# Optimization experiments

Hardware: AMD Instinct MI355X
Metric: run time of the kernel (lower is better)

Reference implementation:

```python
import jax, jax.numpy as jnp
import numpy as np

B, T, C = 2, 2048, 1024
H, D = 16, 64          # n_heads, head_dim
E, K, HD = 8, 2, 1536  # num_experts, active_experts, expert hidden (int(1.5*C))
EPS = 1e-6


def setup_inputs() -> dict:
    key = jax.random.key(0)
    ks = jax.random.split(key, 13)
    s = 0.02
    return {
        "x": jax.random.normal(ks[0], (B, T, C), jnp.float32),
        "rope_cos": jax.random.uniform(ks[1], (T, D), jnp.float32),
        "rope_sin": jax.random.uniform(ks[2], (T, D), jnp.float32),
        "attn_norm_w": jnp.ones((C,), jnp.float32),
        "q_w": jax.random.normal(ks[3], (C, C), jnp.float32) * s,
        "k_w": jax.random.normal(ks[4], (C, C), jnp.float32) * s,
        "v_w": jax.random.normal(ks[5], (C, C), jnp.float32) * s,
        "o_w": jax.random.normal(ks[6], (C, C), jnp.float32) * s,
        "ffn_norm_w": jnp.ones((C,), jnp.float32),
        "router_w": jax.random.normal(ks[7], (E, C), jnp.float32) * s,
        "w1": jax.random.normal(ks[8], (E, HD, C), jnp.float32) * s,
        "w2": jax.random.normal(ks[9], (E, C, HD), jnp.float32) * s,
        "w3": jax.random.normal(ks[10], (E, HD, C), jnp.float32) * s,
    }


def rmsnorm(x, w):
    var = jnp.mean(x * x, axis=-1, keepdims=True)
    return w * x * jax.lax.rsqrt(var + EPS)


def apply_rope(x, cos, sin):
    # x: [B, T, H, D]; cos/sin: [T, D]
    cos = cos[None, :, None, :]
    sin = sin[None, :, None, :]
    d = x.shape[-1] // 2
    x1, x2 = x[..., :d], x[..., d:]
    rotated = jnp.concatenate([-x2, x1], axis=-1)
    return x * cos + rotated * sin


def reference(x, rope_cos, rope_sin, attn_norm_w, q_w, k_w, v_w, o_w,
              ffn_norm_w, router_w, w1, w2, w3):
    b, t, c = x.shape
    h = rmsnorm(x, attn_norm_w)
    q = (h @ q_w.T).reshape(b, t, H, D)
    k = (h @ k_w.T).reshape(b, t, H, D)
    v = (h @ v_w.T).reshape(b, t, H, D)
    q = apply_rope(q, rope_cos[:t], rope_sin[:t]).transpose(0, 2, 1, 3)  # [B,H,T,D]
    k = apply_rope(k, rope_cos[:t], rope_sin[:t]).transpose(0, 2, 1, 3)
    v = v.transpose(0, 2, 1, 3)
    scores = jnp.einsum('bhqd,bhkd->bhqk', q, k) / jnp.sqrt(jnp.asarray(D, q.dtype))
    causal = jnp.tril(jnp.ones((t, t), bool))
    scores = jnp.where(causal, scores, -jnp.inf)
    attn = jax.nn.softmax(scores, axis=-1)
    y = jnp.einsum('bhqk,bhkd->bhqd', attn, v)
    y = y.transpose(0, 2, 1, 3).reshape(b, t, c)
    x = x + y @ o_w.T

    # Sparse MoE (top-K routing, per-expert SwiGLU, weighted combine)
    hn = rmsnorm(x, ffn_norm_w)
    flat = hn.reshape(-1, c)                                # [N, C]
    logits = flat @ router_w.T                              # [N, E]
    wk, idx = jax.lax.top_k(logits, K)                      # [N, K]
    wk = jax.nn.softmax(wk, axis=-1)
    # combined per-expert gate: [N, E] (zero for unrouted experts)
    gate = jnp.sum((idx[..., None] == jnp.arange(E)) * wk[..., None], axis=1)
    out = jnp.zeros_like(flat)
    for e in range(E):
        g = jax.nn.silu(flat @ w1[e].T) * (flat @ w3[e].T)  # [N, HD]
        out = out + gate[:, e:e + 1] * (g @ w2[e].T)
    return x + out.reshape(b, t, c)
```

## Files before the change

### kernel.cpp

```cpp
#include <hip/hip_runtime.h>
#include <hip/hip_bf16.h>
#include <math.h>

#define Bq 2
#define Tq 2048
#define Cq 1024
#define Hq 16
#define Dq 64
#define Eq 8
#define HDq 1536
#define NTOK (Bq*Tq)

typedef unsigned short u16;
typedef _Float16 f16;
typedef __bf16 bf16x8 __attribute__((ext_vector_type(8)));
typedef _Float16 f16x8 __attribute__((ext_vector_type(8)));
typedef float f32x4v __attribute__((ext_vector_type(4)));

#define MB(x) ((size_t)(x) * 262144)

__device__ __forceinline__ float silu_f(float a) {
    return a / (1.0f + __expf(-a));
}
__device__ __forceinline__ u16 f2bf(float f) {
    union { float f; unsigned u; } a; a.f = f;
    unsigned r = a.u + 0x7fffu + ((a.u >> 16) & 1u);
    return (u16)(r >> 16);
}
__device__ __forceinline__ u16 f16bits(f16 h) {
    union { f16 f; u16 u; } a; a.f = h; return a.u;
}

__device__ __forceinline__ void stage16(const void* g, void* l) {
    __builtin_amdgcn_global_load_lds(
        (const __attribute__((address_space(1))) unsigned int*)g,
        (__attribute__((address_space(3))) unsigned int*)l, 16, 0, 0);
}

__global__ __launch_bounds__(256) void rmsnorm_split_k(const float* __restrict__ x,
                                                       const float* __restrict__ w,
                                                       u16* __restrict__ hh,
                                                       u16* __restrict__ hl) {
    int row = blockIdx.x;
    int tid = threadIdx.x;
    const float* xr = x + (size_t)row * Cq;
    float4 v = *(const float4*)(xr + tid * 4);
    float ss = v.x*v.x + v.y*v.y + v.z*v.z + v.w*v.w;
    #pragma unroll
    for (int off = 32; off; off >>= 1) ss += __shfl_xor(ss, off);
    __shared__ float red[4];
    if ((tid & 63) == 0) red[tid >> 6] = ss;
    __syncthreads();
    float tot = red[0] + red[1] + red[2] + red[3];
    float scale = rsqrtf(tot * (1.0f / (float)Cq) + 1e-6f);
    float4 wv = *(const float4*)(w + tid * 4);
    float o[4] = { v.x*wv.x*scale, v.y*wv.y*scale, v.z*wv.z*scale, v.w*wv.w*scale };
    ushort4 oh, ol;
    u16* ph = (u16*)&oh; u16* pl = (u16*)&ol;
    #pragma unroll
    for (int i = 0; i < 4; i++) {
        f16 hi = (f16)o[i]; f16 lo = (f16)(o[i] - (float)hi);
        ph[i] = f16bits(hi); pl[i] = f16bits(lo);
    }
    *(ushort4*)(hh + (size_t)row * Cq + tid * 4) = oh;
    *(ushort4*)(hl + (size_t)row * Cq + tid * 4) = ol;
}

__global__ __launch_bounds__(256) void rmsnorm2_k(const float* __restrict__ x,
                                                  const float* __restrict__ w,
                                                  float* __restrict__ hn,
                                                  u16* __restrict__ hnb) {
    int row = blockIdx.x;
    int tid = threadIdx.x;
    const float* xr = x + (size_t)row * Cq;
    float4 v = *(const float4*)(xr + tid * 4);
    float ss = v.x*v.x + v.y*v.y + v.z*v.z + v.w*v.w;
    #pragma unroll
    for (int off = 32; off; off >>= 1) ss += __shfl_xor(ss, off);
    __shared__ float red[4];
    if ((tid & 63) == 0) red[tid >> 6] = ss;
    __syncthreads();
    float tot = red[0] + red[1] + red[2] + red[3];
    float scale = rsqrtf(tot * (1.0f / (float)Cq) + 1e-6f);
    float4 wv = *(const float4*)(w + tid * 4);
    float4 o = make_float4(v.x*wv.x*scale, v.y*wv.y*scale, v.z*wv.z*scale, v.w*wv.w*scale);
    *(float4*)(hn + (size_t)row * Cq + tid * 4) = o;
    ushort4 ob = make_ushort4(f2bf(o.x), f2bf(o.y), f2bf(o.z), f2bf(o.w));
    *(ushort4*)(hnb + (size_t)row * Cq + tid * 4) = ob;
}

__global__ __launch_bounds__(256) void wconv_k(const float* __restrict__ w1,
                                               const float* __restrict__ w3,
                                               const float* __restrict__ w2,
                                               u16* __restrict__ w1b,
                                               u16* __restrict__ w3b,
                                               u16* __restrict__ w2b) {
    int a = blockIdx.y;
    const float* src = (a == 0) ? w1 : ((a == 1) ? w3 : w2);
    u16* dst = (a == 0) ? w1b : ((a == 1) ? w3b : w2b);
    size_t i = ((size_t)blockIdx.x * 256 + threadIdx.x) * 8;
    float4 f0 = *(const float4*)(src + i);
    float4 f1 = *(const float4*)(src + i + 4);
    ushort4 o0 = make_ushort4(f2bf(f0.x), f2bf(f0.y), f2bf(f0.z), f2bf(f0.w));
    ushort4 o1 = make_ushort4(f2bf(f1.x), f2bf(f1.y), f2bf(f1.z), f2bf(f1.w));
    *(ushort4*)(dst + i)     = o0;
    *(ushort4*)(dst + i + 4) = o1;
}

__global__ __launch_bounds__(256, 3) void gemm_fused(const u16* __restrict__ Ahg,
                                                     const u16* __restrict__ Alg,
                                                     const float* __restrict__ Wq,
                                                     const float* __restrict__ Wk,
                                                     const float* __restrict__ Wv,
                                                     u16* __restrict__ qh_o,
                                                     u16* __restrict__ ql_o,
                                                     u16* __restrict__ kh_o,
                                                     u16* __restrict__ kl_o,
                                                     float* __restrict__ vf_o,
                                                     const float* __restrict__ cosb,
                                                     const float* __restrict__ sinb,
                                                     const float* __restrict__ aux,
                                                     float* __restrict__ outf,
                                                     int kind) {
    __shared__ u16 AhS[2][128*32], AlS[2][128*32], BhS[128*32], BlS[128*32];
    int tid = threadIdx.x;
    int wave = tid >> 6, lane = tid & 63;
    int wm = wave >> 1, wn = wave & 1;
    int bx = blockIdx.x, by = blockIdx.y;
    int proj, nx;
    const float* W;
    if (kind == 0) {
        proj = bx >> 3; nx = bx & 7;
        W = (proj == 0) ? Wq : ((proj == 1) ? Wk : Wv);
    } else {
        proj = 3; nx = bx; W = Wq;
    }

    int srow = tid >> 2, sch = (tid & 3) * 8;
    const u16* A0 = Ahg + (size_t)(by*128 + srow) * Cq + sch;
    const u16* A1 = A0 + (size_t)64 * Cq;
    const u16* L0 = Alg + (size_t)(by*128 + srow) * Cq + sch;
    const u16* L1 = L0 + (size_t)64 * Cq;
    const float* W0 = W + (size_t)(nx*128 + srow) * Cq + sch;
    const float* W1 = W0 + (size_t)64 * Cq;
    int lo0 = srow*32 + sch, lo1 = lo0 + 2048;

    f32x4v acc[4][4];
    #pragma unroll
    for (int i = 0; i < 4; i++)
        #pragma unroll
        for (int j = 0; j < 4; j++)
            #pragma unroll
            for (int r = 0; r < 4; r++) acc[i][j][r] = 0.0f;

    float wr0[8], wr1[8];
    stage16(A0, &AhS[0][lo0]);
    stage16(A1, &AhS[0][lo1]);
    stage16(L0, &AlS[0][lo0]);
    stage16(L1, &AlS[0][lo1]);
    *(float4*)&wr0[0] = *(const float4*)(W0);
    *(float4*)&wr0[4] = *(const float4*)(W0 + 4);
    *(float4*)&wr1[0] = *(const float4*)(W1);
    *(float4*)&wr1[4] = *(const float4*)(W1 + 4);

    int fr = lane & 15, fk = (lane >> 4) * 8;
    int cur = 0;
    for (int k0 = 0; k0 < Cq; k0 += 32, cur ^= 1) {
        __syncthreads();
        {
            f16x8 bh0, bl0, bh1, bl1;
            #pragma unroll
            for (int i = 0; i < 8; i++) {
                f16 h0 = (f16)wr0[i]; bh0[i] = h0; bl0[i] = (f16)(wr0[i] - (float)h0);
                f16 h1 = (f16)wr1[i]; bh1[i] = h1; bl1[i] = (f16)(wr1[i] - (float)h1);
            }
            *(f16x8*)(void*)&BhS[lo0] = bh0;
            *(f16x8*)(void*)&BlS[lo0] = bl0;
            *(f16x8*)(void*)&BhS[lo1] = bh1;
            *(f16x8*)(void*)&BlS[lo1] = bl1;
        }
        __syncthreads();
        int kn = k0 + 32;
        if (kn < Cq) {
            stage16(A0 + kn, &AhS[cur^1][lo0]);
            stage16(A1 + kn, &AhS[cur^1][lo1]);
            stage16(L0 + kn, &AlS[cur^1][lo0]);
            stage16(L1 + kn, &AlS[cur^1][lo1]);
            *(float4*)&wr0[0] = *(const float4*)(W0 + kn);
            *(float4*)&wr0[4] = *(const float4*)(W0 + kn + 4);
            *(float4*)&wr1[0] = *(const float4*)(W1 + kn);
            *(float4*)&wr1[4] = *(const float4*)(W1 + kn + 4);
        }
        f16x8 ah[4], al[4];
        #pragma unroll
        for (int mi = 0; mi < 4; mi++) {
            ah[mi] = *(const f16x8*)(const void*)&AhS[cur][(wm*64 + mi*16 + fr)*32 + fk];
            al[mi] = *(const f16x8*)(const void*)&AlS[cur][(wm*64 + mi*16 + fr)*32 + fk];
        }
        #pragma unroll
        for (int ni = 0; ni < 4; ni++) {
            f16x8 bhf = *(const f16x8*)(const void*)&BhS[(wn*64 + ni*16 + fr)*32 + fk];
            f16x8 blf = *(const f16x8*)(const void*)&BlS[(wn*64 + ni*16 + fr)*32 + fk];
            #pragma unroll
            for (int mi = 0; mi < 4; mi++) {
                acc[mi][ni] = __builtin_amdgcn_mfma_f32_16x16x32_f16(ah[mi], bhf, acc[mi][ni], 0, 0, 0);
                acc[mi][ni] = __builtin_amdgcn_mfma_f32_16x16x32_f16(ah[mi], blf, acc[mi][ni], 0, 0, 0);
                acc[mi][ni] = __builtin_amdgcn_mfma_f32_16x16x32_f16(al[mi], bhf, acc[mi][ni], 0, 0, 0);
            }
        }
    }

    int cr = (lane >> 4) * 4, cc = lane & 15;
    if (proj < 2) {
        u16* dh = (proj == 0) ? qh_o : kh_o;
        u16* dl = (proj == 0) ? ql_o : kl_o;
        float scale = (proj == 0) ? 0.125f : 1.0f;
        int hd = (nx * 2 + wn) * 64;
        #pragma unroll
        for (int mi = 0; mi < 4; mi++)
            #pragma unroll
            for (int r = 0; r < 4; r++) {
                int row = by*128 + wm*64 + mi*16 + cr + r;
                int t = row & (Tq - 1);
                #pragma unroll
                for (int ni = 0; ni < 2; ni++) {
                    int d0 = ni*16 + cc;
                    float a = acc[mi][ni][r];
                    float b = acc[mi][ni+2][r];
                    float c0 = cosb[t*Dq + d0],      s0 = sinb[t*Dq + d0];
                    float c1 = cosb[t*Dq + d0 + 32], s1 = sinb[t*Dq + d0 + 32];
                    float oa = (a * c0 - b * s0) * scale;
                    float ob = (b * c1 + a * s1) * scale;
                    size_t off = (size_t)row * Cq + hd + d0;
                    f16 ha = (f16)oa;
                    f16 hb = (f16)ob;
                    dh[off]      = f16bits(ha);
                    dl[off]      = f16bits((f16)(oa - (float)ha));
                    dh[off + 32] = f16bits(hb);
                    dl[off + 32] = f16bits((f16)(ob - (float)hb));
                }
            }
    } else if (proj == 2) {
        #pragma unroll
        for (int mi = 0; mi < 4; mi++)
            #pragma unroll
            for (int r = 0; r < 4; r++) {
                int row = by*128 + wm*64 + mi*16 + cr + r;
                #pragma unroll
                for (int ni = 0; ni < 4; ni++)
                    vf_o[(size_t)row * Cq + nx*128 + wn*64 + ni*16 + cc] = acc[mi][ni][r];
            }
    } else {
        #pragma unroll
        for (int mi = 0; mi < 4; mi++)
            #pragma unroll
            for (int r = 0; r < 4; r++) {
                int row = by*128 + wm*64 + mi*16 + cr + r;
                #pragma unroll
                for (int ni = 0; ni < 4; ni++) {
                    size_t off = (size_t)row * Cq + nx*128 + wn*64 + ni*16 + cc;
                    outf[off] = acc[mi][ni][r] + aux[off];
                }
            }
    }
}

__global__ __launch_bounds__(256) void vtrans_k(const float* __restrict__ v,
                                                u16* __restrict__ vth,
                                                u16* __restrict__ vtl) {
    __shared__ u16 Th[64 * 72];
    __shared__ u16 Tl[64 * 72];
    int tc = blockIdx.x;
    int bh = blockIdx.y;
    int b = bh >> 4, h = bh & 15;
    int tid = threadIdx.x;
    int tr = tid >> 2;
    int dc = (tid & 3) * 16;
    size_t gin = ((size_t)(b * Tq + tc * 64 + tr)) * Cq + h * Dq + dc;
    #pragma unroll
    for (int i = 0; i < 16; i += 4) {
        float4 f = *(const float4*)(v + gin + i);
        float fv[4] = {f.x, f.y, f.z, f.w};
        #pragma unroll
        for (int j = 0; j < 4; j++) {
            f16 hi = (f16)fv[j];
            f16 lo = (f16)(fv[j] - (float)hi);
            Th[(dc + i + j) * 72 + tr] = f16bits(hi);
            Tl[(dc + i + j) * 72 + tr] = f16bits(lo);
        }
    }
    __syncthreads();
    int dr = tid >> 2;
    int cc = (tid & 3) * 16;
    size_t gout = ((size_t)(bh * 64 + dr)) * Tq + tc * 64 + cc;
    *(uint4*)(vth + gout)     = *(uint4*)(Th + dr * 72 + cc);
    *(uint4*)(vth + gout + 8) = *(uint4*)(Th + dr * 72 + cc + 8);
    *(uint4*)(vtl + gout)     = *(uint4*)(Tl + dr * 72 + cc);
    *(uint4*)(vtl + gout + 8) = *(uint4*)(Tl + dr * 72 + cc + 8);
}

#define AST 72
__global__ __launch_bounds__(256, 2) void attn_f16(const u16* __restrict__ qh_g,
                                                   const u16* __restrict__ ql_g,
                                                   const u16* __restrict__ kh_g,
                                                   const u16* __restrict__ kl_g,
                                                   const u16* __restrict__ vth_g,
                                                   const u16* __restrict__ vtl_g,
                                                   u16* __restrict__ yh_g,
                                                   u16* __restrict__ yl_g) {
    __shared__ u16 Qh[64*AST], Ql[64*AST];
    __shared__ u16 Kh[64*AST], Kl[64*AST];
    __shared__ u16 Vh[64*AST], Vl[64*AST];
    __shared__ u16 Ph[64*AST], Pl[64*AST];

    int j  = blockIdx.x;
    int bh = blockIdx.y;
    int b = bh >> 4, h = bh & 15;
    int tid = threadIdx.x;
    int wv = tid >> 6, lane = tid & 63;
    int fr = lane & 15, fg = lane >> 4;
    int sr = tid >> 2, sc = (tid & 3) * 16;
    int aoff = (wv * 16 + fr) * AST + fg * 8;

    uint4 rkh0, rkh1, rkl0, rkl1, rvh0, rvh1, rvl0, rvl1;
    auto ldkv = [&](int kt) {
        size_t kg = ((size_t)(b * Tq + kt * 64 + sr)) * Cq + h * Dq + sc;
        size_t vg = ((size_t)(bh * 64 + sr)) * Tq + kt * 64 + sc;
        rkh0 = *(const uint4*)(kh_g + kg);  rkh1 = *(const uint4*)(kh_g + kg + 8);
        rkl0 = *(const uint4*)(kl_g + kg);  rkl1 = *(const uint4*)(kl_g + kg + 8);
        rvh0 = *(const uint4*)(vth_g + vg); rvh1 = *(const uint4*)(vth_g + vg + 8);
        rvl0 = *(const uint4*)(vtl_g + vg); rvl1 = *(const uint4*)(vtl_g + vg + 8);
    };

    #pragma unroll
    for (int pass = 0; pass < 2; pass++) {
        int qt = pass == 0 ? (31 - j) : j;

        __syncthreads();
        {
            size_t g = ((size_t)(b * Tq + qt * 64 + sr)) * Cq + h * Dq + sc;
            *(uint4*)(Qh + sr*AST + sc)     = *(const uint4*)(qh_g + g);
            *(uint4*)(Qh + sr*AST + sc + 8) = *(const uint4*)(qh_g + g + 8);
            *(uint4*)(Ql + sr*AST + sc)     = *(const uint4*)(ql_g + g);
            *(uint4*)(Ql + sr*AST + sc + 8) = *(const uint4*)(ql_g + g + 8);
        }
        ldkv(0);

        f32x4v acc_o[4];
        float m_i[4], l_i[4];
        #pragma unroll
        for (int i = 0; i < 4; i++) {
            m_i[i] = -1e30f; l_i[i] = 0.0f;
            #pragma unroll
            for (int r = 0; r < 4; r++) acc_o[i][r] = 0.0f;
        }

        for (int kt = 0; kt <= qt; kt++) {
            __syncthreads();
            *(uint4*)(Kh + sr*AST + sc)     = rkh0;
            *(uint4*)(Kh + sr*AST + sc + 8) = rkh1;
            *(uint4*)(Kl + sr*AST + sc)     = rkl0;
            *(uint4*)(Kl + sr*AST + sc + 8) = rkl1;
            *(uint4*)(Vh + sr*AST + sc)     = rvh0;
            *(uint4*)(Vh + sr*AST + sc + 8) = rvh1;
            *(uint4*)(Vl + sr*AST + sc)     = rvl0;
            *(uint4*)(Vl + sr*AST + sc + 8) = rvl1;
            __syncthreads();
            if (kt < qt) ldkv(kt + 1);

            f16x8 aqh0 = *(const f16x8*)(const void*)(Qh + aoff);
            f16x8 aqh1 = *(const f16x8*)(const void*)(Qh + aoff + 32);
            f16x8 aql0 = *(const f16x8*)(const void*)(Ql + aoff);
            f16x8 aql1 = *(const f16x8*)(const void*)(Ql + aoff + 32);

            f32x4v s[4];
            #pragma unroll
            for (int ni = 0; ni < 4; ni++) {
                int boff = (ni * 16 + fr) * AST + fg * 8;
                f16x8 kh0 = *(const f16x8*)(const void*)(Kh + boff);
                f16x8 kh1 = *(const f16x8*)(const void*)(Kh + boff + 32);
                f16x8 kl0 = *(const f16x8*)(const void*)(Kl + boff);
                f16x8 kl1 = *(const f16x8*)(const void*)(Kl + boff + 32);
                f32x4v t;
                #pragma unroll
                for (int r = 0; r < 4; r++) t[r] = 0.0f;
                t = __builtin_amdgcn_mfma_f32_16x16x32_f16(aqh0, kh0, t, 0, 0, 0);
                t = __builtin_amdgcn_mfma_f32_16x16x32_f16(aqh1, kh1, t, 0, 0, 0);
                t = __builtin_amdgcn_mfma_f32_16x16x32_f16(aqh0, kl0, t, 0, 0, 0);
                t = __builtin_amdgcn_mfma_f32_16x16x32_f16(aqh1, kl1, t, 0, 0, 0);
                t = __builtin_amdgcn_mfma_f32_16x16x32_f16(aql0, kh0, t, 0, 0, 0);
                t = __builtin_amdgcn_mfma_f32_16x16x32_f16(aql1, kh1, t, 0, 0, 0);
                s[ni] = t;
            }

            if (kt == qt) {
                #pragma unroll
                for (int ni = 0; ni < 4; ni++) {
                    int col = ni * 16 + fr;
                    #pragma unroll
                    for (int r = 0; r < 4; r++) {
                        int row = wv * 16 + fg * 4 + r;
                        if (col > row) s[ni][r] = -1e30f;
                    }
                }
            }

            float p[4][4];
            #pragma unroll
            for (int r = 0; r < 4; r++) {
                float mx = fmaxf(fmaxf(s[0][r], s[1][r]), fmaxf(s[2][r], s[3][r]));
                #pragma unroll
                for (int off = 1; off < 16; off <<= 1)
                    mx = fmaxf(mx, __shfl_xor(mx, off, 16));
                float mn = fmaxf(m_i[r], mx);
                float rs = 0.0f;
                #pragma unroll
                for (int ni = 0; ni < 4; ni++) {
                    p[ni][r] = __expf(s[ni][r] - mn);
                    rs += p[ni][r];
                }
                #pragma unroll
                for (int off = 1; off < 16; off <<= 1)
                    rs += __shfl_xor(rs, off, 16);
                float alpha = __expf(m_i[r] - mn);
                l_i[r] = l_i[r] * alpha + rs;
                m_i[r] = mn;
                #pragma unroll
                for (int ni = 0; ni < 4; ni++) acc_o[ni][r] *= alpha;
            }

            #pragma unroll
            for (int ni = 0; ni < 4; ni++) {
                #pragma unroll
                for (int r = 0; r < 4; r++) {
                    int off = (wv * 16 + fg * 4 + r) * AST + ni * 16 + fr;
                    f16 ph = (f16)p[ni][r];
                    f16 pl = (f16)(p[ni][r] - (float)ph);
                    Ph[off] = f16bits(ph);
                    Pl[off] = f16bits(pl);
                }
            }

            f16x8 aph0 = *(const f16x8*)(const void*)(Ph + aoff);
            f16x8 aph1 = *(const f16x8*)(const void*)(Ph + aoff + 32);
            f16x8 apl0 = *(const f16x8*)(const void*)(Pl + aoff);
            f16x8 apl1 = *(const f16x8*)(const void*)(Pl + aoff + 32);
            #pragma unroll
            for (int ni = 0; ni < 4; ni++) {
                int boff = (ni * 16 + fr) * AST + fg * 8;
                f16x8 vh0 = *(const f16x8*)(const void*)(Vh + boff);
                f16x8 vh1 = *(const f16x8*)(const void*)(Vh + boff + 32);
                f16x8 vl0 = *(const f16x8*)(const void*)(Vl + boff);
                f16x8 vl1 = *(const f16x8*)(const void*)(Vl + boff + 32);
                f32x4v t = acc_o[ni];
                t = __builtin_amdgcn_mfma_f32_16x16x32_f16(aph0, vh0, t, 0, 0, 0);
                t = __builtin_amdgcn_mfma_f32_16x16x32_f16(aph1, vh1, t, 0, 0, 0);
                t = __builtin_amdgcn_mfma_f32_16x16x32_f16(aph0, vl0, t, 0, 0, 0);
                t = __builtin_amdgcn_mfma_f32_16x16x32_f16(aph1, vl1, t, 0, 0, 0);
                t = __builtin_amdgcn_mfma_f32_16x16x32_f16(apl0, vh0, t, 0, 0, 0);
                t = __builtin_amdgcn_mfma_f32_16x16x32_f16(apl1, vh1, t, 0, 0, 0);
                acc_o[ni] = t;
            }
        }

        #pragma unroll
        for (int r = 0; r < 4; r++) {
            float inv = 1.0f / l_i[r];
            int row = qt * 64 + wv * 16 + fg * 4 + r;
            size_t base = ((size_t)(b * Tq + row)) * Cq + h * Dq + fr;
            #pragma unroll
            for (int ni = 0; ni < 4; ni++) {
                float yv = acc_o[ni][r] * inv;
                f16 hi = (f16)yv;
                f16 lo = (f16)(yv - (float)hi);
                yh_g[base + ni * 16] = f16bits(hi);
                yl_g[base + ni * 16] = f16bits(lo);
            }
        }
    }
}

__global__ void zero_k(int* cnt) {
    if (threadIdx.x < Eq) cnt[threadIdx.x] = 0;
}

__global__ __launch_bounds__(64) void router_k(const float* __restrict__ hn,
                                               const float* __restrict__ rw,
                                               int* __restrict__ cnt,
                                               int* __restrict__ idxl,
                                               float* __restrict__ gvl) {
    int tkn = blockIdx.x;
    int lane = threadIdx.x;
    float acc[Eq] = {};
    for (int it = 0; it < Cq / 64; it++) {
        float hv = hn[(size_t)tkn * Cq + it * 64 + lane];
        #pragma unroll
        for (int e = 0; e < Eq; e++)
            acc[e] = fmaf(hv, rw[e * Cq + it * 64 + lane], acc[e]);
    }
    #pragma unroll
    for (int e = 0; e < Eq; e++) {
        #pragma unroll
        for (int off = 32; off; off >>= 1) acc[e] += __shfl_xor(acc[e], off);
    }
    int i0 = 0;
    #pragma unroll
    for (int e = 1; e < Eq; e++) if (acc[e] > acc[i0]) i0 = e;
    int i1 = (i0 == 0) ? 1 : 0;
    #pragma unroll
    for (int e = 0; e < Eq; e++)
        if (e != i0 && acc[e] > acc[i1]) i1 = e;
    float p1 = __expf(acc[i1] - acc[i0]);
    float g0 = 1.0f / (1.0f + p1);
    float g1 = p1 / (1.0f + p1);
    if (lane == 0) {
        int p0 = atomicAdd(&cnt[i0], 1);
        idxl[i0 * NTOK + p0] = tkn;
        gvl[i0 * NTOK + p0] = g0;
        int p1i = atomicAdd(&cnt[i1], 1);
        idxl[i1 * NTOK + p1i] = tkn;
        gvl[i1 * NTOK + p1i] = g1;
    }
}

__global__ void setup_k(const int* __restrict__ cnt, int* __restrict__ seg,
                        int* __restrict__ texp, int* __restrict__ ttot) {
    if (threadIdx.x == 0) {
        int base = 0;
        for (int e = 0; e < Eq; e++) {
            seg[e] = base * 128;
            int t = (cnt[e] + 127) >> 7;
            for (int i = 0; i < t; i++) texp[base + i] = e;
            base += t;
        }
        *ttot = base;
    }
}

__global__ __launch_bounds__(256, 2) void moe_w13b(const u16* __restrict__ hnb,
                                                   const u16* __restrict__ w1b,
                                                   const u16* __restrict__ w3b,
                                                   u16* __restrict__ gbuf,
                                                   const int* __restrict__ cnt,
                                                   const int* __restrict__ seg,
                                                   const int* __restrict__ texp,
                                                   const int* __restrict__ ttot,
                                                   const int* __restrict__ idxl) {
    int by = blockIdx.y;
    if (by >= *ttot) return;
    int e = texp[by];
    const u16* w1e = w1b + (size_t)e * HDq * Cq;
    const u16* w3e = w3b + (size_t)e * HDq * Cq;
    int cnte = cnt[e], sege = seg[e];
    const int* idxe = idxl + e * NTOK;

    __shared__ u16 As[2][128*32], B1S[2][128*32], B3S[2][128*32];
    int tid = threadIdx.x;
    int wave = tid >> 6, lane = tid & 63;
    int wm = wave >> 1, wn = wave & 1;
    int bx = blockIdx.x;
    int srow = tid >> 2, sch = (tid & 3) * 8;

    int r0 = by*128 + srow, r1 = r0 + 64;
    int li0 = r0 - sege, li1 = r1 - sege;
    int tok0 = idxe[li0 < cnte ? li0 : 0];
    int tok1 = idxe[li1 < cnte ? li1 : 0];
    const u16* A0 = hnb + (size_t)tok0 * Cq + sch;
    const u16* A1 = hnb + (size_t)tok1 * Cq + sch;
    const u16* W10 = w1e + (size_t)(bx*128 + srow) * Cq + sch;
    const u16* W11 = W10 + (size_t)64 * Cq;
    const u16* W30 = w3e + (size_t)(bx*128 + srow) * Cq + sch;
    const u16* W31 = W30 + (size_t)64 * Cq;
    int lo0 = srow*32 + sch, lo1 = lo0 + 2048;

    f32x4v acc1[4][4], acc3[4][4];
    #pragma unroll
    for (int i = 0; i < 4; i++)
        #pragma unroll
        for (int j = 0; j < 4; j++)
            #pragma unroll
            for (int r = 0; r < 4; r++) { acc1[i][j][r] = 0.0f; acc3[i][j][r] = 0.0f; }

    stage16(A0,  &As[0][lo0]);  stage16(A1,  &As[0][lo1]);
    stage16(W10, &B1S[0][lo0]); stage16(W11, &B1S[0][lo1]);
    stage16(W30, &B3S[0][lo0]); stage16(W31, &B3S[0][lo1]);

    int fr = lane & 15, fk = (lane >> 4) * 8;
    int cur = 0;
    for (int k0 = 0; k0 < Cq; k0 += 32, cur ^= 1) {
        __syncthreads();
        int kn = k0 + 32;
        if (kn < Cq) {
            stage16(A0 + kn,  &As[cur^1][lo0]);  stage16(A1 + kn,  &As[cur^1][lo1]);
            stage16(W10 + kn, &B1S[cur^1][lo0]); stage16(W11 + kn, &B1S[cur^1][lo1]);
            stage16(W30 + kn, &B3S[cur^1][lo0]); stage16(W31 + kn, &B3S[cur^1][lo1]);
        }
        bf16x8 af[4];
        #pragma unroll
        for (int mi = 0; mi < 4; mi++)
            af[mi] = *(const bf16x8*)&As[cur][(wm*64 + mi*16 + fr) * 32 + fk];
        #pragma unroll
        for (int ni = 0; ni < 4; ni++) {
            bf16x8 b1f = *(const bf16x8*)&B1S[cur][(wn*64 + ni*16 + fr) * 32 + fk];
            bf16x8 b3f = *(const bf16x8*)&B3S[cur][(wn*64 + ni*16 + fr) * 32 + fk];
            #pragma unroll
            for (int mi = 0; mi < 4; mi++) {
                acc1[mi][ni] = __builtin_amdgcn_mfma_f32_16x16x32_bf16(af[mi], b1f, acc1[mi][ni], 0, 0, 0);
                acc3[mi][ni] = __builtin_amdgcn_mfma_f32_16x16x32_bf16(af[mi], b3f, acc3[mi][ni], 0, 0, 0);
            }
        }
    }

    int cr = (lane >> 4) * 4, cc = lane & 15;
    #pragma unroll
    for (int mi = 0; mi < 4; mi++)
        #pragma unroll
        for (int ni = 0; ni < 4; ni++)
            #pragma unroll
            for (int r = 0; r < 4; r++) {
                int row = by*128 + wm*64 + mi*16 + cr + r;
                int col = bx*128 + wn*64 + ni*16 + cc;
                gbuf[(size_t)row * HDq + col] = f2bf(silu_f(acc1[mi][ni][r]) * acc3[mi][ni][r]);
            }
}

__global__ __launch_bounds__(256, 3) void moe_w2b_k(const u16* __restrict__ gbuf,
                                                    const u16* __restrict__ w2b,
                                                    float* __restrict__ out,
                                                    const int* __restrict__ cnt,
                                                    const int* __restrict__ seg,
                                                    const int* __restrict__ texp,
                                                    const int* __restrict__ ttot,
                                                    const int* __restrict__ idxl,
                                                    const float* __restrict__ gvl) {
    int by = blockIdx.y;
    if (by >= *ttot) return;
    int e = texp[by];
    const u16* w2e = w2b + (size_t)e * Cq * HDq;
    int cnte = cnt[e], sege = seg[e];
    const int* idxe = idxl + e * NTOK;
    const float* gve = gvl + e * NTOK;

    __shared__ u16 As[2][128*32], Bs[2][128*32];
    int tid = threadIdx.x;
    int wave = tid >> 6, lane = tid & 63;
    int wm = wave >> 1, wn = wave & 1;
    int bx = blockIdx.x;
    int srow = tid >> 2, sch = (tid & 3) * 8;

    const u16* A0 = gbuf + (size_t)(by*128 + srow) * HDq + sch;
    const u16* A1 = A0 + (size_t)64 * HDq;
    const u16* W0 = w2e + (size_t)(bx*128 + srow) * HDq + sch;
    const u16* W1 = W0 + (size_t)64 * HDq;
    int lo0 = srow*32 + sch, lo1 = lo0 + 2048;

    f32x4v acc[4][4];
    #pragma unroll
    for (int i = 0; i < 4; i++)
        #pragma unroll
        for (int j = 0; j < 4; j++)
            #pragma unroll
            for (int r = 0; r < 4; r++) acc[i][j][r] = 0.0f;

    stage16(A0, &As[0][lo0]); stage16(A1, &As[0][lo1]);
    stage16(W0, &Bs[0][lo0]); stage16(W1, &Bs[0][lo1]);

    int fr = lane & 15, fk = (lane >> 4) * 8;
    int cur = 0;
    for (int k0 = 0; k0 < HDq; k0 += 32, cur ^= 1) {
        __syncthreads();
        int kn = k0 + 32;
        if (kn < HDq) {
            stage16(A0 + kn, &As[cur^1][lo0]); stage16(A1 + kn, &As[cur^1][lo1]);
            stage16(W0 + kn, &Bs[cur^1][lo0]); stage16(W1 + kn, &Bs[cur^1][lo1]);
        }
        bf16x8 af[4];
        #pragma unroll
        for (int mi = 0; mi < 4; mi++)
            af[mi] = *(const bf16x8*)&As[cur][(wm*64 + mi*16 + fr) * 32 + fk];
        #pragma unroll
        for (int ni = 0; ni < 4; ni++) {
            bf16x8 bf_ = *(const bf16x8*)&Bs[cur][(wn*64 + ni*16 + fr) * 32 + fk];
            #pragma unroll
            for (int mi = 0; mi < 4; mi++)
                acc[mi][ni] = __builtin_amdgcn_mfma_f32_16x16x32_bf16(af[mi], bf_, acc[mi][ni], 0, 0, 0);
        }
    }

    int cr = (lane >> 4) * 4, cc = lane & 15;
    #pragma unroll
    for (int mi = 0; mi < 4; mi++)
        #pragma unroll
        for (int r = 0; r < 4; r++) {
            int row = by*128 + wm*64 + mi*16 + cr + r;
            int local = row - sege;
            if (local < cnte) {
                int token = idxe[local];
                float g = gve[local];
                #pragma unroll
                for (int ni = 0; ni < 4; ni++) {
                    int col = bx*128 + wn*64 + ni*16 + cc;
                    atomicAdd(&out[(size_t)token * Cq + col], g * acc[mi][ni][r]);
                }
            }
        }
}

__global__ __launch_bounds__(256, 2) void moe_w13(const u16* __restrict__ hnb,
                                                  const float* __restrict__ w1,
                                                  const float* __restrict__ w3,
                                                  u16* __restrict__ gbuf,
                                                  const int* __restrict__ cnt,
                                                  const int* __restrict__ seg,
                                                  const int* __restrict__ texp,
                                                  const int* __restrict__ ttot,
                                                  const int* __restrict__ idxl) {
    int by = blockIdx.y;
    if (by >= *ttot) return;
    int e = texp[by];
    const float* w1e = w1 + (size_t)e * HDq * Cq;
    const float* w3e = w3 + (size_t)e * HDq * Cq;
    int cnte = cnt[e], sege = seg[e];
    const int* idxe = idxl + e * NTOK;

    __shared__ u16 As[2][128*32], B1S[128*32], B3S[128*32];
    int tid = threadIdx.x;
    int wave = tid >> 6, lane = tid & 63;
    int wm = wave >> 1, wn = wave & 1;
    int bx = blockIdx.x;
    int srow = tid >> 2, sch = (tid & 3) * 8;

    int r0 = by*128 + srow, r1 = r0 + 64;
    int li0 = r0 - sege, li1 = r1 - sege;
    int tok0 = idxe[li0 < cnte ? li0 : 0];
    int tok1 = idxe[li1 < cnte ? li1 : 0];
    const u16* A0 = hnb + (size_t)tok0 * Cq + sch;
    const u16* A1 = hnb + (size_t)tok1 * Cq + sch;
    const float* W10 = w1e + (size_t)(bx*128 + srow) * Cq + sch;
    const float* W11 = W10 + (size_t)64 * Cq;
    const float* W30 = w3e + (size_t)(bx*128 + srow) * Cq + sch;
    const float* W31 = W30 + (size_t)64 * Cq;
    int lo0 = srow*32 + sch, lo1 = lo0 + 2048;

    f32x4v acc1[4][4], acc3[4][4];
    #pragma unroll
    for (int i = 0; i < 4; i++)
        #pragma unroll
        for (int j = 0; j < 4; j++)
            #pragma unroll
            for (int r = 0; r < 4; r++) { acc1[i][j][r] = 0.0f; acc3[i][j][r] = 0.0f; }

    float x1a[8], x1b[8], x3a[8], x3b[8];
    stage16(A0, &As[0][lo0]);
    stage16(A1, &As[0][lo1]);
    *(float4*)&x1a[0] = *(const float4*)(W10);
    *(float4*)&x1a[4] = *(const float4*)(W10 + 4);
    *(float4*)&x1b[0] = *(const float4*)(W11);
    *(float4*)&x1b[4] = *(const float4*)(W11 + 4);
    *(float4*)&x3a[0] = *(const float4*)(W30);
    *(float4*)&x3a[4] = *(const float4*)(W30 + 4);
    *(float4*)&x3b[0] = *(const float4*)(W31);
    *(float4*)&x3b[4] = *(const float4*)(W31 + 4);

    int fr = lane & 15, fk = (lane >> 4) * 8;
    int cur = 0;
    for (int k0 = 0; k0 < Cq; k0 += 32, cur ^= 1) {
        __syncthreads();
        {
            u16 t0[8], t1[8], t2[8], t3[8];
            #pragma unroll
            for (int i = 0; i < 8; i++) {
                t0[i] = f2bf(x1a[i]); t1[i] = f2bf(x1b[i]);
                t2[i] = f2bf(x3a[i]); t3[i] = f2bf(x3b[i]);
            }
            *(uint4*)&B1S[lo0] = *(uint4*)t0;
            *(uint4*)&B1S[lo1] = *(uint4*)t1;
            *(uint4*)&B3S[lo0] = *(uint4*)t2;
            *(uint4*)&B3S[lo1] = *(uint4*)t3;
        }
        __syncthreads();
        int kn = k0 + 32;
        if (kn < Cq) {
            stage16(A0 + kn, &As[cur^1][lo0]);
            stage16(A1 + kn, &As[cur^1][lo1]);
            *(float4*)&x1a[0] = *(const float4*)(W10 + kn);
            *(float4*)&x1a[4] = *(const float4*)(W10 + kn + 4);
            *(float4*)&x1b[0] = *(const float4*)(W11 + kn);
            *(float4*)&x1b[4] = *(const float4*)(W11 + kn + 4);
            *(float4*)&x3a[0] = *(const float4*)(W30 + kn);
            *(float4*)&x3a[4] = *(const float4*)(W30 + kn + 4);
            *(float4*)&x3b[0] = *(const float4*)(W31 + kn);
            *(float4*)&x3b[4] = *(const float4*)(W31 + kn + 4);
        }
        bf16x8 af[4];
        #pragma unroll
        for (int mi = 0; mi < 4; mi++)
            af[mi] = *(const bf16x8*)&As[cur][(wm*64 + mi*16 + fr) * 32 + fk];
        #pragma unroll
        for (int ni = 0; ni < 4; ni++) {
            bf16x8 b1f = *(const bf16x8*)&B1S[(wn*64 + ni*16 + fr) * 32 + fk];
            bf16x8 b3f = *(const bf16x8*)&B3S[(wn*64 + ni*16 + fr) * 32 + fk];
            #pragma unroll
            for (int mi = 0; mi < 4; mi++) {
                acc1[mi][ni] = __builtin_amdgcn_mfma_f32_16x16x32_bf16(af[mi], b1f, acc1[mi][ni], 0, 0, 0);
                acc3[mi][ni] = __builtin_amdgcn_mfma_f32_16x16x32_bf16(af[mi], b3f, acc3[mi][ni], 0, 0, 0);
            }
        }
    }

    int cr = (lane >> 4) * 4, cc = lane & 15;
    #pragma unroll
    for (int mi = 0; mi < 4; mi++)
        #pragma unroll
        for (int ni = 0; ni < 4; ni++)
            #pragma unroll
            for (int r = 0; r < 4; r++) {
                int row = by*128 + wm*64 + mi*16 + cr + r;
                int col = bx*128 + wn*64 + ni*16 + cc;
                gbuf[(size_t)row * HDq + col] = f2bf(silu_f(acc1[mi][ni][r]) * acc3[mi][ni][r]);
            }
}

__global__ __launch_bounds__(256, 3) void moe_w2(const u16* __restrict__ gbuf,
                                                 const float* __restrict__ w2,
                                                 float* __restrict__ out,
                                                 const int* __restrict__ cnt,
                                                 const int* __restrict__ seg,
                                                 const int* __restrict__ texp,
                                                 const int* __restrict__ ttot,
                                                 const int* __restrict__ idxl,
                                                 const float* __restrict__ gvl) {
    int by = blockIdx.y;
    if (by >= *ttot) return;
    int e = texp[by];
    const float* w2e = w2 + (size_t)e * Cq * HDq;
    int cnte = cnt[e], sege = seg[e];
    const int* idxe = idxl + e * NTOK;
    const float* gve = gvl + e * NTOK;

    __shared__ u16 As[2][128*32], Bs[128*32];
    int tid = threadIdx.x;
    int wave = tid >> 6, lane = tid & 63;
    int wm = wave >> 1, wn = wave & 1;
    int bx = blockIdx.x;
    int srow = tid >> 2, sch = (tid & 3) * 8;

    const u16* A0 = gbuf + (size_t)(by*128 + srow) * HDq + sch;
    const u16* A1 = A0 + (size_t)64 * HDq;
    const float* W0 = w2e + (size_t)(bx*128 + srow) * HDq + sch;
    const float* W1 = W0 + (size_t)64 * HDq;
    int lo0 = srow*32 + sch, lo1 = lo0 + 2048;

    f32x4v acc[4][4];
    #pragma unroll
    for (int i = 0; i < 4; i++)
        #pragma unroll
        for (int j = 0; j < 4; j++)
            #pragma unroll
            for (int r = 0; r < 4; r++) acc[i][j][r] = 0.0f;

    float xa[8], xb[8];
    stage16(A0, &As[0][lo0]);
    stage16(A1, &As[0][lo1]);
    *(float4*)&xa[0] = *(const float4*)(W0);
    *(float4*)&xa[4] = *(const float4*)(W0 + 4);
    *(float4*)&xb[0] = *(const float4*)(W1);
    *(float4*)&xb[4] = *(const float4*)(W1 + 4);

    int fr = lane & 15, fk = (lane >> 4) * 8;
    int cur = 0;
    for (int k0 = 0; k0 < HDq; k0 += 32, cur ^= 1) {
        __syncthreads();
        {
            u16 ta[8], tb[8];
            #pragma unroll
            for (int i = 0; i < 8; i++) { ta[i] = f2bf(xa[i]); tb[i] = f2bf(xb[i]); }
            *(uint4*)&Bs[lo0] = *(uint4*)ta;
            *(uint4*)&Bs[lo1] = *(uint4*)tb;
        }
        __syncthreads();
        int kn = k0 + 32;
        if (kn < HDq) {
            stage16(A0 + kn, &As[cur^1][lo0]);
            stage16(A1 + kn, &As[cur^1][lo1]);
            *(float4*)&xa[0] = *(const float4*)(W0 + kn);
            *(float4*)&xa[4] = *(const float4*)(W0 + kn + 4);
            *(float4*)&xb[0] = *(const float4*)(W1 + kn);
            *(float4*)&xb[4] = *(const float4*)(W1 + kn + 4);
        }
        bf16x8 af[4];
        #pragma unroll
        for (int mi = 0; mi < 4; mi++)
            af[mi] = *(const bf16x8*)&As[cur][(wm*64 + mi*16 + fr) * 32 + fk];
        #pragma unroll
        for (int ni = 0; ni < 4; ni++) {
            bf16x8 bf_ = *(const bf16x8*)&Bs[(wn*64 + ni*16 + fr) * 32 + fk];
            #pragma unroll
            for (int mi = 0; mi < 4; mi++)
                acc[mi][ni] = __builtin_amdgcn_mfma_f32_16x16x32_bf16(af[mi], bf_, acc[mi][ni], 0, 0, 0);
        }
    }

    int cr = (lane >> 4) * 4, cc = lane & 15;
    #pragma unroll
    for (int mi = 0; mi < 4; mi++)
        #pragma unroll
        for (int r = 0; r < 4; r++) {
            int row = by*128 + wm*64 + mi*16 + cr + r;
            int local = row - sege;
            if (local < cnte) {
                int token = idxe[local];
                float g = gve[local];
                #pragma unroll
                for (int ni = 0; ni < 4; ni++) {
                    int col = bx*128 + wn*64 + ni*16 + cc;
                    atomicAdd(&out[(size_t)token * Cq + col], g * acc[mi][ni][r]);
                }
            }
        }
}

extern "C" void kernel_launch(void* const* d_in, const int* in_sizes, int n_in,
                              void* d_out, int out_size, void* d_ws, size_t ws_size,
                              hipStream_t stream) {
    (void)in_sizes; (void)n_in; (void)out_size;

    const float* x     = (const float*)d_in[0];
    const float* ropec = (const float*)d_in[1];
    const float* ropes = (const float*)d_in[2];
    const float* anw   = (const float*)d_in[3];
    const float* q_w   = (const float*)d_in[4];
    const float* k_w   = (const float*)d_in[5];
    const float* v_w   = (const float*)d_in[6];
    const float* o_w   = (const float*)d_in[7];
    const float* fnw   = (const float*)d_in[8];
    const float* rtw   = (const float*)d_in[9];
    const float* w1    = (const float*)d_in[10];
    const float* w2    = (const float*)d_in[11];
    const float* w3    = (const float*)d_in[12];
    float* out = (float*)d_out;

    float* ws = (float*)d_ws;
    u16* hh = (u16*)(ws + MB(0));
    u16* hl = (u16*)(ws + MB(8));
    float* vf = ws + MB(16);
    u16* qh = (u16*)(ws + MB(32));
    u16* ql = (u16*)(ws + MB(40));
    u16* kh = (u16*)(ws + MB(48));
    u16* kl = (u16*)(ws + MB(56));
    u16* vth = (u16*)(ws + MB(0));
    u16* vtl = (u16*)(ws + MB(8));
    u16* yh  = (u16*)(ws + MB(16));
    u16* yl  = (u16*)(ws + MB(24));
    u16* gbuf = (u16*)(ws + MB(0));
    float* hn = ws + MB(32);
    u16* hnb  = (u16*)(ws + MB(48));
    int* cntp = (int*)(ws + MB(56));
    int* segp = cntp + 8;
    int* texp = cntp + 16;
    int* ttot = cntp + 96;
    int* idxl = cntp + 256;
    float* gvl = (float*)(cntp + 256 + Eq*NTOK);
    u16* w1b = (u16*)(ws + MB(64));
    u16* w3b = (u16*)(ws + MB(88));
    u16* w2b = (u16*)(ws + MB(112));

    const int M = NTOK;
    const bool pre = ws_size >= ((size_t)136 << 20);

    if (pre)
        hipLaunchKernelGGL(wconv_k, dim3(6144, 3), dim3(256), 0, stream,
                           w1, w3, w2, w1b, w3b, w2b);

    hipLaunchKernelGGL(rmsnorm_split_k, dim3(M), dim3(256), 0, stream, x, anw, hh, hl);

    hipLaunchKernelGGL(gemm_fused, dim3(24, M/128), dim3(256), 0, stream,
                       hh, hl, q_w, k_w, v_w, qh, ql, kh, kl, vf,
                       ropec, ropes, (const float*)nullptr, (float*)nullptr, 0);

    hipLaunchKernelGGL(vtrans_k, dim3(32, 32), dim3(256), 0, stream, vf, vth, vtl);

    hipLaunchKernelGGL(attn_f16, dim3(16, Bq*Hq), dim3(256), 0, stream,
                       qh, ql, kh, kl, vth, vtl, yh, yl);

    hipLaunchKernelGGL(gemm_fused, dim3(8, M/128), dim3(256), 0, stream,
                       yh, yl, o_w, (const float*)nullptr, (const float*)nullptr,
                       (u16*)nullptr, (u16*)nullptr, (u16*)nullptr, (u16*)nullptr,
                       (float*)nullptr, ropec, ropes, x, out, 1);

    hipLaunchKernelGGL(rmsnorm2_k, dim3(M), dim3(256), 0, stream, out, fnw, hn, hnb);

    hipLaunchKernelGGL(zero_k, dim3(1), dim3(64), 0, stream, cntp);
    hipLaunchKernelGGL(router_k, dim3(M), dim3(64), 0, stream, hn, rtw, cntp, idxl, gvl);
    hipLaunchKernelGGL(setup_k, dim3(1), dim3(64), 0, stream, cntp, segp, texp, ttot);

    if (pre) {
        hipLaunchKernelGGL(moe_w13b, dim3(HDq/128, 72), dim3(256), 0, stream,
                           hnb, w1b, w3b, gbuf, cntp, segp, texp, ttot, idxl);
        hipLaunchKernelGGL(moe_w2b_k, dim3(Cq/128, 72), dim3(256), 0, stream,
                           gbuf, w2b, out, cntp, segp, texp, ttot, idxl, gvl);
    } else {
        hipLaunchKernelGGL(moe_w13, dim3(HDq/128, 72), dim3(256), 0, stream,
                           hnb, w1, w3, gbuf, cntp, segp, texp, ttot, idxl);
        hipLaunchKernelGGL(moe_w2, dim3(Cq/128, 72), dim3(256), 0, stream,
                           gbuf, w2, out, cntp, segp, texp, ttot, idxl, gvl);
    }
}
```

Baseline: 721.1 us.

## Pre-split attention weights into f16 hi/lo and stream them via double buffering

Adds a kernel that converts the Q/K/V/O fp32 weights once per call into f16 hi/lo pairs, plus a new GEMM that loads these pre-split weights with double-buffered shared memory. The old path split the weights inside each GEMM tile. The attention grid is flattened so blocks interleave across heads, and the P tile stride changes to reduce LDS bank conflicts. The new path runs only when the workspace is large enough. It adds an extra launch and 16MB of workspace traffic, and the double-buffered B tiles raise LDS use, which lowers occupancy to 2 blocks.

```diff
diff --git a/kernel.cpp b/kernel.cpp
--- a/kernel.cpp
+++ b/kernel.cpp
@@ -105,6 +105,32 @@
     ushort4 o1 = make_ushort4(f2bf(f1.x), f2bf(f1.y), f2bf(f1.z), f2bf(f1.w));
     *(ushort4*)(dst + i)     = o0;
     *(ushort4*)(dst + i + 4) = o1;
+}
+
+__global__ __launch_bounds__(256) void wsplit_k(const float* __restrict__ qw,
+                                                const float* __restrict__ kw,
+                                                const float* __restrict__ vw,
+                                                const float* __restrict__ ow,
+                                                u16* __restrict__ qhp, u16* __restrict__ qlp,
+                                                u16* __restrict__ khp, u16* __restrict__ klp,
+                                                u16* __restrict__ vhp, u16* __restrict__ vlp,
+                                                u16* __restrict__ ohp, u16* __restrict__ olp) {
+    int a = blockIdx.y;
+    const float* src = (a == 0) ? qw : ((a == 1) ? kw : ((a == 2) ? vw : ow));
+    u16* dh = (a == 0) ? qhp : ((a == 1) ? khp : ((a == 2) ? vhp : ohp));
+    u16* dl = (a == 0) ? qlp : ((a == 1) ? klp : ((a == 2) ? vlp : olp));
+    size_t i = ((size_t)blockIdx.x * 256 + threadIdx.x) * 8;
+    float f[8];
+    *(float4*)&f[0] = *(const float4*)(src + i);
+    *(float4*)&f[4] = *(const float4*)(src + i + 4);
+    u16 oh[8], ol[8];
+    #pragma unroll
+    for (int j = 0; j < 8; j++) {
+        f16 hi = (f16)f[j]; f16 lo = (f16)(f[j] - (float)hi);
+        oh[j] = f16bits(hi); ol[j] = f16bits(lo);
+    }
+    *(uint4*)(dh + i) = *(uint4*)oh;
+    *(uint4*)(dl + i) = *(uint4*)ol;
 }
 
 __global__ __launch_bounds__(256, 3) void gemm_fused(const u16* __restrict__ Ahg,
@@ -265,6 +291,148 @@
     }
 }
 
+__global__ __launch_bounds__(256, 2) void gemm_fused2(const u16* __restrict__ Ahg,
+                                                      const u16* __restrict__ Alg,
+                                                      const u16* __restrict__ Bh0,
+                                                      const u16* __restrict__ Bl0,
+                                                      const u16* __restrict__ Bh1,
+                                                      const u16* __restrict__ Bl1,
+                                                      const u16* __restrict__ Bh2,
+                                                      const u16* __restrict__ Bl2,
+                                                      u16* __restrict__ qh_o,
+                                                      u16* __restrict__ ql_o,
+                                                      u16* __restrict__ kh_o,
+                                                      u16* __restrict__ kl_o,
+                                                      float* __restrict__ vf_o,
+                                                      const float* __restrict__ cosb,
+                                                      const float* __restrict__ sinb,
+                                                      const float* __restrict__ aux,
+                                                      float* __restrict__ outf,
+                                                      int kind) {
+    __shared__ u16 AhS[2][128*32], AlS[2][128*32], BhS[2][128*32], BlS[2][128*32];
+    int tid = threadIdx.x;
+    int wave = tid >> 6, lane = tid & 63;
+    int wm = wave >> 1, wn = wave & 1;
+    int bx = blockIdx.x, by = blockIdx.y;
+    int proj, nx;
+    const u16 *Bh, *Bl;
+    if (kind == 0) {
+        proj = bx >> 3; nx = bx & 7;
+        Bh = (proj == 0) ? Bh0 : ((proj == 1) ? Bh1 : Bh2);
+        Bl = (proj == 0) ? Bl0 : ((proj == 1) ? Bl1 : Bl2);
+    } else {
+        proj = 3; nx = bx; Bh = Bh0; Bl = Bl0;
+    }
+
+    int srow = tid >> 2, sch = (tid & 3) * 8;
+    const u16* A0 = Ahg + (size_t)(by*128 + srow) * Cq + sch;
+    const u16* A1 = A0 + (size_t)64 * Cq;
+    const u16* L0 = Alg + (size_t)(by*128 + srow) * Cq + sch;
+    const u16* L1 = L0 + (size_t)64 * Cq;
+    const u16* H0 = Bh + (size_t)(nx*128 + srow) * Cq + sch;
+    const u16* H1 = H0 + (size_t)64 * Cq;
+    const u16* G0 = Bl + (size_t)(nx*128 + srow) * Cq + sch;
+    const u16* G1 = G0 + (size_t)64 * Cq;
+    int lo0 = srow*32 + sch, lo1 = lo0 + 2048;
+
+    f32x4v acc[4][4];
+    #pragma unroll
+    for (int i = 0; i < 4; i++)
+        #pragma unroll
+        for (int j = 0; j < 4; j++)
+            #pragma unroll
+            for (int r = 0; r < 4; r++) acc[i][j][r] = 0.0f;
+
+    stage16(A0, &AhS[0][lo0]); stage16(A1, &AhS[0][lo1]);
+    stage16(L0, &AlS[0][lo0]); stage16(L1, &AlS[0][lo1]);
+    stage16(H0, &BhS[0][lo0]); stage16(H1, &BhS[0][lo1]);
+    stage16(G0, &BlS[0][lo0]); stage16(G1, &BlS[0][lo1]);
+
+    int fr = lane & 15, fk = (lane >> 4) * 8;
+    int cur = 0;
+    for (int k0 = 0; k0 < Cq; k0 += 32, cur ^= 1) {
+        __syncthreads();
+        int kn = k0 + 32;
+        if (kn < Cq) {
+            stage16(A0 + kn, &AhS[cur^1][lo0]); stage16(A1 + kn, &AhS[cur^1][lo1]);
+            stage16(L0 + kn, &AlS[cur^1][lo0]); stage16(L1 + kn, &AlS[cur^1][lo1]);
+            stage16(H0 + kn, &BhS[cur^1][lo0]); stage16(H1 + kn, &BhS[cur^1][lo1]);
+            stage16(G0 + kn, &BlS[cur^1][lo0]); stage16(G1 + kn, &BlS[cur^1][lo1]);
+        }
+        f16x8 ah[4], al[4];
+        #pragma unroll
+        for (int mi = 0; mi < 4; mi++) {
+            ah[mi] = *(const f16x8*)(const void*)&AhS[cur][(wm*64 + mi*16 + fr)*32 + fk];
+            al[mi] = *(const f16x8*)(const void*)&AlS[cur][(wm*64 + mi*16 + fr)*32 + fk];
+        }
+        #pragma unroll
+        for (int ni = 0; ni < 4; ni++) {
+            f16x8 bhf = *(const f16x8*)(const void*)&BhS[cur][(wn*64 + ni*16 + fr)*32 + fk];
+            f16x8 blf = *(const f16x8*)(const void*)&BlS[cur][(wn*64 + ni*16 + fr)*32 + fk];
+            #pragma unroll
+            for (int mi = 0; mi < 4; mi++) {
+                acc[mi][ni] = __builtin_amdgcn_mfma_f32_16x16x32_f16(ah[mi], bhf, acc[mi][ni], 0, 0, 0);
+                acc[mi][ni] = __builtin_amdgcn_mfma_f32_16x16x32_f16(ah[mi], blf, acc[mi][ni], 0, 0, 0);
+                acc[mi][ni] = __builtin_amdgcn_mfma_f32_16x16x32_f16(al[mi], bhf, acc[mi][ni], 0, 0, 0);
+            }
+        }
+    }
+
+    int cr = (lane >> 4) * 4, cc = lane & 15;
+    if (proj < 2) {
+        u16* dh = (proj == 0) ? qh_o : kh_o;
+        u16* dl = (proj == 0) ? ql_o : kl_o;
+        float scale = (proj == 0) ? 0.125f : 1.0f;
+        int hd = (nx * 2 + wn) * 64;
+        #pragma unroll
+        for (int mi = 0; mi < 4; mi++)
+            #pragma unroll
+            for (int r = 0; r < 4; r++) {
+                int row = by*128 + wm*64 + mi*16 + cr + r;
+                int t = row & (Tq - 1);
+                #pragma unroll
+                for (int ni = 0; ni < 2; ni++) {
+                    int d0 = ni*16 + cc;
+                    float a = acc[mi][ni][r];
+                    float b = acc[mi][ni+2][r];
+                    float c0 = cosb[t*Dq + d0],      s0 = sinb[t*Dq + d0];
+                    float c1 = cosb[t*Dq + d0 + 32], s1 = sinb[t*Dq + d0 + 32];
+                    float oa = (a * c0 - b * s0) * scale;
+                    float ob = (b * c1 + a * s1) * scale;
+                    size_t off = (size_t)row * Cq + hd + d0;
+                    f16 ha = (f16)oa;
+                    f16 hb = (f16)ob;
+                    dh[off]      = f16bits(ha);
+                    dl[off]      = f16bits((f16)(oa - (float)ha));
+                    dh[off + 32] = f16bits(hb);
+                    dl[off + 32] = f16bits((f16)(ob - (float)hb));
+                }
+            }
+    } else if (proj == 2) {
+        #pragma unroll
+        for (int mi = 0; mi < 4; mi++)
+            #pragma unroll
+            for (int r = 0; r < 4; r++) {
+                int row = by*128 + wm*64 + mi*16 + cr + r;
+                #pragma unroll
+                for (int ni = 0; ni < 4; ni++)
+                    vf_o[(size_t)row * Cq + nx*128 + wn*64 + ni*16 + cc] = acc[mi][ni][r];
+            }
+    } else {
+        #pragma unroll
+        for (int mi = 0; mi < 4; mi++)
+            #pragma unroll
+            for (int r = 0; r < 4; r++) {
+                int row = by*128 + wm*64 + mi*16 + cr + r;
+                #pragma unroll
+                for (int ni = 0; ni < 4; ni++) {
+                    size_t off = (size_t)row * Cq + nx*128 + wn*64 + ni*16 + cc;
+                    outf[off] = acc[mi][ni][r] + aux[off];
+                }
+            }
+    }
+}
+
 __global__ __launch_bounds__(256) void vtrans_k(const float* __restrict__ v,
                                                 u16* __restrict__ vth,
                                                 u16* __restrict__ vtl) {
@@ -300,6 +468,7 @@
 }
 
 #define AST 72
+#define PST 68
 __global__ __launch_bounds__(256, 2) void attn_f16(const u16* __restrict__ qh_g,
                                                    const u16* __restrict__ ql_g,
                                                    const u16* __restrict__ kh_g,
@@ -311,16 +480,18 @@
     __shared__ u16 Qh[64*AST], Ql[64*AST];
     __shared__ u16 Kh[64*AST], Kl[64*AST];
     __shared__ u16 Vh[64*AST], Vl[64*AST];
-    __shared__ u16 Ph[64*AST], Pl[64*AST];
-
-    int j  = blockIdx.x;
-    int bh = blockIdx.y;
+    __shared__ u16 Ph[64*PST], Pl[64*PST];
+
+    int id = blockIdx.x;
+    int bh = id & 31;
+    int j  = id >> 5;
     int b = bh >> 4, h = bh & 15;
     int tid = threadIdx.x;
     int wv = tid >> 6, lane = tid & 63;
     int fr = lane & 15, fg = lane >> 4;
     int sr = tid >> 2, sc = (tid & 3) * 16;
     int aoff = (wv * 16 + fr) * AST + fg * 8;
+    int poff = (wv * 16 + fr) * PST + fg * 8;
 
     uint4 rkh0, rkh1, rkl0, rkl1, rvh0, rvh1, rvl0, rvl1;
     auto ldkv = [&](int kt) {
@@ -433,7 +604,7 @@
             for (int ni = 0; ni < 4; ni++) {
                 #pragma unroll
                 for (int r = 0; r < 4; r++) {
-                    int off = (wv * 16 + fg * 4 + r) * AST + ni * 16 + fr;
+                    int off = (wv * 16 + fg * 4 + r) * PST + ni * 16 + fr;
                     f16 ph = (f16)p[ni][r];
                     f16 pl = (f16)(p[ni][r] - (float)ph);
                     Ph[off] = f16bits(ph);
@@ -441,10 +612,10 @@
                 }
             }
 
-            f16x8 aph0 = *(const f16x8*)(const void*)(Ph + aoff);
-            f16x8 aph1 = *(const f16x8*)(const void*)(Ph + aoff + 32);
-            f16x8 apl0 = *(const f16x8*)(const void*)(Pl + aoff);
-            f16x8 apl1 = *(const f16x8*)(const void*)(Pl + aoff + 32);
+            f16x8 aph0 = *(const f16x8*)(const void*)(Ph + poff);
+            f16x8 aph1 = *(const f16x8*)(const void*)(Ph + poff + 32);
+            f16x8 apl0 = *(const f16x8*)(const void*)(Pl + poff);
+            f16x8 apl1 = *(const f16x8*)(const void*)(Pl + poff + 32);
             #pragma unroll
             for (int ni = 0; ni < 4; ni++) {
                 int boff = (ni * 16 + fr) * AST + fg * 8;
@@ -964,29 +1135,56 @@
     u16* w1b = (u16*)(ws + MB(64));
     u16* w3b = (u16*)(ws + MB(88));
     u16* w2b = (u16*)(ws + MB(112));
+    u16* wqh = (u16*)(ws + MB(136));
+    u16* wql = (u16*)(ws + MB(138));
+    u16* wkh = (u16*)(ws + MB(140));
+    u16* wkl = (u16*)(ws + MB(142));
+    u16* wvh = (u16*)(ws + MB(144));
+    u16* wvl = (u16*)(ws + MB(146));
+    u16* woh = (u16*)(ws + MB(148));
+    u16* wol = (u16*)(ws + MB(150));
 
     const int M = NTOK;
-    const bool pre = ws_size >= ((size_t)136 << 20);
+    const bool pre  = ws_size >= ((size_t)136 << 20);
+    const bool pre2 = ws_size >= ((size_t)152 << 20);
 
     if (pre)
         hipLaunchKernelGGL(wconv_k, dim3(6144, 3), dim3(256), 0, stream,
                            w1, w3, w2, w1b, w3b, w2b);
+    if (pre2)
+        hipLaunchKernelGGL(wsplit_k, dim3(512, 4), dim3(256), 0, stream,
+                           q_w, k_w, v_w, o_w,
+                           wqh, wql, wkh, wkl, wvh, wvl, woh, wol);
 
     hipLaunchKernelGGL(rmsnorm_split_k, dim3(M), dim3(256), 0, stream, x, anw, hh, hl);
 
-    hipLaunchKernelGGL(gemm_fused, dim3(24, M/128), dim3(256), 0, stream,
-                       hh, hl, q_w, k_w, v_w, qh, ql, kh, kl, vf,
-                       ropec, ropes, (const float*)nullptr, (float*)nullptr, 0);
+    if (pre2)
+        hipLaunchKernelGGL(gemm_fused2, dim3(24, M/128), dim3(256), 0, stream,
+                           hh, hl, wqh, wql, wkh, wkl, wvh, wvl,
+                           qh, ql, kh, kl, vf,
+                           ropec, ropes, (const float*)nullptr, (float*)nullptr, 0);
+    else
+        hipLaunchKernelGGL(gemm_fused, dim3(24, M/128), dim3(256), 0, stream,
+                           hh, hl, q_w, k_w, v_w, qh, ql, kh, kl, vf,
+                           ropec, ropes, (const float*)nullptr, (float*)nullptr, 0);
 
     hipLaunchKernelGGL(vtrans_k, dim3(32, 32), dim3(256), 0, stream, vf, vth, vtl);
 
-    hipLaunchKernelGGL(attn_f16, dim3(16, Bq*Hq), dim3(256), 0, stream,
+    hipLaunchKernelGGL(attn_f16, dim3(512), dim3(256), 0, stream,
                        qh, ql, kh, kl, vth, vtl, yh, yl);
 
-    hipLaunchKernelGGL(gemm_fused, dim3(8, M/128), dim3(256), 0, stream,
-                       yh, yl, o_w, (const float*)nullptr, (const float*)nullptr,
-                       (u16*)nullptr, (u16*)nullptr, (u16*)nullptr, (u16*)nullptr,
-                       (float*)nullptr, ropec, ropes, x, out, 1);
+    if (pre2)
+        hipLaunchKernelGGL(gemm_fused2, dim3(8, M/128), dim3(256), 0, stream,
+                           yh, yl, woh, wol,
+                           (const u16*)nullptr, (const u16*)nullptr,
+                           (const u16*)nullptr, (const u16*)nullptr,
+                           (u16*)nullptr, (u16*)nullptr, (u16*)nullptr, (u16*)nullptr,
+                           (float*)nullptr, ropec, ropes, x, out, 1);
+    else
+        hipLaunchKernelGGL(gemm_fused, dim3(8, M/128), dim3(256), 0, stream,
+                           yh, yl, o_w, (const float*)nullptr, (const float*)nullptr,
+                           (u16*)nullptr, (u16*)nullptr, (u16*)nullptr, (u16*)nullptr,
+                           (float*)nullptr, ropec, ropes, x, out, 1);
 
     hipLaunchKernelGGL(rmsnorm2_k, dim3(M), dim3(256), 0, stream, out, fnw, hn, hnb);
 
```

Result: slower. 757.5 us (+5.0%).
